# Kernel tuning notes

Hardware: AMD Instinct MI355X
Metric: run time of the kernel (lower is better)

Reference implementation:

```python
import jax, jax.numpy as jnp
import numpy as np

N, E, D, H, LAYERS = 50000, 800000, 128, 8, 2
LRELU_ALPHA = 0.2


def _seg_softmax(logits, seg, n):
    # numerically stable softmax over edges grouped by destination node
    m = jax.ops.segment_max(logits, seg, num_segments=n)
    z = jnp.exp(logits - m[seg])
    s = jax.ops.segment_sum(z, seg, num_segments=n)
    return z / jnp.maximum(s[seg], 1e-16)


def _gat_layer(x, src, dst, W, a_src, a_dst, concat):
    # W: [H, Fin, F'], a_src/a_dst: [H, F']
    n = x.shape[0]
    outs = []
    for h in range(W.shape[0]):  # loop over heads to bound peak memory
        Wh = x @ W[h]                              # [N, F']
        es = Wh @ a_src[h]                         # [N]
        ed = Wh @ a_dst[h]                         # [N]
        e = jax.nn.leaky_relu(es[src] + ed[dst], LRELU_ALPHA)  # [E]
        att = _seg_softmax(e, dst, n)              # [E]
        out = jax.ops.segment_sum(att[:, None] * Wh[src], dst, num_segments=n)
        outs.append(out)
    if concat:
        return jax.nn.elu(jnp.concatenate(outs, axis=-1))  # [N, H*F']
    return jnp.mean(jnp.stack(outs, axis=0), axis=0)        # [N, F']


def _rel_gcn_layer(x, src, dst, w, W):
    # weighted-adjacency GCN with row (in-degree) normalization + ReLU
    n = x.shape[0]
    deg = jax.ops.segment_sum(w, dst, num_segments=n)
    norm = w / jnp.maximum(deg[dst], 1e-16)        # [E]
    h = x @ W                                      # [N, Dout]
    agg = jax.ops.segment_sum(norm[:, None] * h[src], dst, num_segments=n)
    return jax.nn.relu(agg)


def setup_inputs() -> dict:
    key = jax.random.key(0)
    ks = jax.random.split(key, 12)
    s = 1.0 / np.sqrt(D)
    return {
        "x": jax.random.normal(ks[0], (N, D), dtype=jnp.float32),
        "edge_index": jax.random.randint(ks[1], (2, E), 0, N, dtype=jnp.int64),
        "edge_weight": jax.random.uniform(ks[2], (E,), dtype=jnp.float32),
        "gat_W0": jax.random.normal(ks[3], (H, D, D // H), dtype=jnp.float32) * s,
        "gat_a0_src": jax.random.normal(ks[4], (H, D // H), dtype=jnp.float32) * s,
        "gat_a0_dst": jax.random.normal(ks[5], (H, D // H), dtype=jnp.float32) * s,
        "gat_W1": jax.random.normal(ks[6], (H, D, D), dtype=jnp.float32) * s,
        "gat_a1_src": jax.random.normal(ks[7], (H, D), dtype=jnp.float32) * s,
        "gat_a1_dst": jax.random.normal(ks[8], (H, D), dtype=jnp.float32) * s,
        "gcn_W0": jax.random.normal(ks[9], (D, D), dtype=jnp.float32) * s,
        "gcn_W1": jax.random.normal(ks[10], (D, D), dtype=jnp.float32) * s,
    }


def reference(x, edge_index, edge_weight, gat_W0, gat_a0_src, gat_a0_dst,
              gat_W1, gat_a1_src, gat_a1_dst, gcn_W0, gcn_W1):
    src, dst = edge_index[0], edge_index[1]
    gat_params = [(gat_W0, gat_a0_src, gat_a0_dst), (gat_W1, gat_a1_src, gat_a1_dst)]
    gcn_params = [gcn_W0, gcn_W1]
    x1, x2 = x, x  # dropout is identity in eval mode
    for i in range(LAYERS):
        W, a_s, a_d = gat_params[i]
        x1 = _gat_layer(x1, src, dst, W, a_s, a_d, concat=(i != LAYERS - 1))
        x2 = _rel_gcn_layer(x2, src, dst, edge_weight, gcn_params[i])
    # cat along new last dim then MaxPool1d(2) == elementwise max of branches
    return jnp.maximum(x1, x2)
```

## Files before the change

### kernel.cpp

```cpp
#include <hip/hip_runtime.h>

#define LRELU_ALPHA 0.2f

typedef __attribute__((ext_vector_type(8))) short short8;
typedef __attribute__((ext_vector_type(4))) float float4v;
typedef __attribute__((ext_vector_type(2))) float f32x2;

__device__ __forceinline__ unsigned short f2bf(float f) {
  union { float f; unsigned u; } x; x.f = f;
  unsigned r = (x.u + 0x7fff + ((x.u >> 16) & 1)) >> 16;
  return (unsigned short)r;
}
__device__ __forceinline__ float bflo(unsigned u) {
  union { unsigned u; float f; } x; x.u = u << 16; return x.f;
}
__device__ __forceinline__ float bfhi(unsigned u) {
  union { unsigned u; float f; } x; x.u = u & 0xffff0000u; return x.f;
}
__device__ __forceinline__ f32x2 bfpair(unsigned u) {
  return (f32x2){bflo(u), bfhi(u)};
}
__device__ __forceinline__ unsigned packbf(float a, float b) {
  return (unsigned)f2bf(a) | ((unsigned)f2bf(b) << 16);
}


__global__ __launch_bounds__(256) void k_count(const int* __restrict__ dst,
                                               int* __restrict__ cnt, int E) {
  int e = blockIdx.x * 256 + threadIdx.x;
  if (e < E) atomicAdd(&cnt[dst[e]], 1);
}

__global__ __launch_bounds__(1024) void k_scan1(const int* __restrict__ cnt,
                                                int* __restrict__ lscan,
                                                int* __restrict__ bsum, int N) {
  __shared__ int sm[1024];
  int t = threadIdx.x;
  int base = blockIdx.x * 1024;
  int v = (base + t < N) ? cnt[base + t] : 0;
  sm[t] = v;
  __syncthreads();
  for (int off = 1; off < 1024; off <<= 1) {
    int x = (t >= off) ? sm[t - off] : 0;
    __syncthreads();
    sm[t] += x;
    __syncthreads();
  }
  if (base + t < N) lscan[base + t] = sm[t] - v;
  if (t == 1023) bsum[blockIdx.x] = sm[1023];
}

__global__ __launch_bounds__(64) void k_scan2(int* __restrict__ bsum,
                                              int* __restrict__ rowptrN, int nb) {
  int t = threadIdx.x;
  int v = (t < nb) ? bsum[t] : 0;
  int orig = v;
  for (int off = 1; off < 64; off <<= 1) {
    int y = __shfl_up(v, off, 64);
    if (t >= off) v += y;
  }
  if (t < nb) bsum[t] = v - orig;
  if (t == 63) *rowptrN = v;
}

__global__ __launch_bounds__(1024) void k_scan3(int* __restrict__ rowptr,
                                                int* __restrict__ cur,
                                                const int* __restrict__ bsum, int N) {
  int i = blockIdx.x * 1024 + threadIdx.x;
  if (i < N) {
    int v = rowptr[i] + bsum[blockIdx.x];
    rowptr[i] = v;
    cur[i] = v;
  }
}

__global__ __launch_bounds__(256) void k_scatter(const int* __restrict__ src,
                                                 const int* __restrict__ dst,
                                                 const float* __restrict__ w,
                                                 const float* __restrict__ logit0,
                                                 int* __restrict__ cur,
                                                 uint2* __restrict__ edata,
                                                 unsigned short* __restrict__ pedge,
                                                 int E) {
  int e = blockIdx.x * 256 + threadIdx.x;
  if (e >= E) return;
  int d = dst[e];
  int s = src[e];
  int p = atomicAdd(&cur[d], 1);
  edata[p] = make_uint2((unsigned)s, __float_as_uint(w[e]));
  float4 es0 = *(const float4*)(logit0 + (size_t)s * 16);
  float4 es1 = *(const float4*)(logit0 + (size_t)s * 16 + 4);
  float4 ed0 = *(const float4*)(logit0 + (size_t)d * 16 + 8);
  float4 ed1 = *(const float4*)(logit0 + (size_t)d * 16 + 12);
  float lg[8] = {es0.x + ed0.x, es0.y + ed0.y, es0.z + ed0.z, es0.w + ed0.w,
                 es1.x + ed1.x, es1.y + ed1.y, es1.z + ed1.z, es1.w + ed1.w};
  unsigned short o[8];
#pragma unroll
  for (int h = 0; h < 8; ++h) {
    float v = lg[h] > 0.f ? lg[h] : LRELU_ALPHA * lg[h];
    o[h] = f2bf(__expf(fminf(v, 80.f)));
  }
  ushort4 q0 = {o[0], o[1], o[2], o[3]};
  ushort4 q1 = {o[4], o[5], o[6], o[7]};
  *(ushort4*)(pedge + (size_t)p * 8) = q0;
  *(ushort4*)(pedge + (size_t)p * 8 + 4) = q1;
}

__global__ __launch_bounds__(256) void k_pack(const float* __restrict__ W0,
                                              const float* __restrict__ a0s,
                                              const float* __restrict__ a0d,
                                              const float* __restrict__ W1,
                                              const float* __restrict__ a1s,
                                              const float* __restrict__ a1d,
                                              const float* __restrict__ gw0,
                                              const float* __restrict__ gw1,
                                              unsigned short* __restrict__ W0catT,
                                              float* __restrict__ logitW,
                                              unsigned short* __restrict__ gw1T,
                                              unsigned short* __restrict__ va1T,
                                              unsigned short* __restrict__ WstackT) {
  int idx = blockIdx.x * 256 + threadIdx.x;
  if (idx < 32768) {
    int n = idx >> 7, k = idx & 127;
    int q = n >> 2, r = n & 3;
    float v;
    if (r < 2) {
      int o = 2 * q + r;
      int h = o >> 4, f = o & 15;
      v = W0[h * 2048 + k * 16 + f];
    } else {
      int j = 2 * q + (r - 2);
      v = gw0[k * 128 + j];
    }
    W0catT[idx] = f2bf(v);
  } else if (idx < 34816) {
    int j = idx - 32768;
    int k = j >> 4, c = j & 15;
    int h = (c < 8) ? c : c - 8;
    const float* a = (c < 8) ? a0s : a0d;
    float s = 0.f;
    for (int f = 0; f < 16; ++f) s += W0[h * 2048 + k * 16 + f] * a[h * 16 + f];
    logitW[j] = s;
  } else if (idx < 51200) {
    int j = idx - 34816;
    int n = j >> 7, k = j & 127;
    gw1T[j] = f2bf(gw1[k * 128 + n]);
  } else if (idx < 53248) {
    int j = idx - 51200;
    int c = j >> 7, k = j & 127;
    int h = c & 7;
    const float* a = (c < 8) ? a1s : a1d;
    float s = 0.f;
    for (int f = 0; f < 128; ++f) s += W1[h * 16384 + k * 128 + f] * a[h * 128 + f];
    va1T[j] = f2bf(s);
  } else if (idx < 184320) {
    int j = idx - 53248;
    int n = j >> 10, kk = j & 1023;
    int h = kk >> 7, k = kk & 127;
    WstackT[j] = f2bf(W1[h * 16384 + k * 128 + n] * 0.125f);
  }
}

__global__ __launch_bounds__(256) void k_prep(const float* __restrict__ x,
                                              const float* __restrict__ logitW,
                                              unsigned short* __restrict__ xb,
                                              float* __restrict__ logit0, int N) {
  __shared__ float sm[16][132];
  __shared__ float sw[2048];
  int t = threadIdx.x;
  int base = blockIdx.x * 16;
  int r = t >> 4, cc = (t & 15) * 8;
  const float* xr = x + (size_t)(base + r) * 128 + cc;
  float4 v0 = *(const float4*)xr;
  float4 v1 = *(const float4*)(xr + 4);
  ushort4 o0 = {f2bf(v0.x), f2bf(v0.y), f2bf(v0.z), f2bf(v0.w)};
  ushort4 o1 = {f2bf(v1.x), f2bf(v1.y), f2bf(v1.z), f2bf(v1.w)};
  *(ushort4*)(xb + (size_t)(base + r) * 128 + cc) = o0;
  *(ushort4*)(xb + (size_t)(base + r) * 128 + cc + 4) = o1;
  *(float4*)&sm[r][cc] = v0;
  *(float4*)&sm[r][cc + 4] = v1;
  *(float4*)&sw[t * 8] = *(const float4*)(logitW + t * 8);
  *(float4*)&sw[t * 8 + 4] = *(const float4*)(logitW + t * 8 + 4);
  __syncthreads();
  int c = t & 15;
  float acc = 0.f;
#pragma unroll
  for (int k = 0; k < 128; ++k) acc += sm[r][k] * sw[k * 16 + c];
  logit0[(size_t)(base + r) * 16 + c] = acc;
}

__global__ __launch_bounds__(256) void k_pedge(const float* __restrict__ logits,
                                               const uint2* __restrict__ edata,
                                               const int* __restrict__ rowptr,
                                               unsigned short* __restrict__ pedge,
                                               float* __restrict__ linv, int N) {
  int wave = threadIdx.x >> 6, lane = threadIdx.x & 63;
  int d = blockIdx.x * 4 + wave;
  if (d >= N) return;
  int j8 = lane >> 3, h = lane & 7;
  float edv = logits[(size_t)d * 16 + 8 + h];
  int beg = rowptr[d], end = rowptr[d + 1];
  float lsum = 0.f;
  for (int ii = beg + j8; ii < end; ii += 8) {
    unsigned s = edata[ii].x;
    float es = logits[(size_t)s * 16 + h];
    float lg = es + edv;
    lg = lg > 0.f ? lg : LRELU_ALPHA * lg;
    float p = __expf(fminf(lg, 80.f));
    lsum += p;
    pedge[(size_t)ii * 8 + h] = f2bf(p);
  }
  lsum += __shfl_xor(lsum, 8, 64);
  lsum += __shfl_xor(lsum, 16, 64);
  lsum += __shfl_xor(lsum, 32, 64);
  if (lane < 8) linv[(size_t)d * 8 + h] = lsum > 0.f ? 1.f / lsum : 0.f;
}

template <int NT, int OUT_BF16, int EPI>
__global__ __launch_bounds__(256) void k_mgemm(const unsigned short* __restrict__ A, int lda,
                                               const unsigned short* __restrict__ BT, int ldb,
                                               void* __restrict__ Cv, int ldc,
                                               const void* __restrict__ aux,
                                               int M, int Ncols, int K) {
  __shared__ unsigned short As[64][64];
  __shared__ unsigned short Bs[NT * 16][64];
  int tid = threadIdx.x;
  int w = tid >> 6, lane = tid & 63;
  int quad = lane >> 4, l16 = lane & 15;
  int row0 = blockIdx.x * 64;
  int c0 = blockIdx.y * (NT * 16);
  float4v acc[NT];
#pragma unroll
  for (int t = 0; t < NT; ++t) acc[t] = (float4v){0.f, 0.f, 0.f, 0.f};

  for (int k0 = 0; k0 < K; k0 += 64) {
    __syncthreads();
#pragma unroll
    for (int i = 0; i < 2; ++i) {
      int c = tid + i * 256;
      int r = c >> 3, kc = c & 7;
      uint4 v = {0u, 0u, 0u, 0u};
      int gr = row0 + r;
      if (gr < M) v = *(const uint4*)(A + (size_t)gr * lda + k0 + kc * 8);
      *(uint4*)(&As[r][(kc ^ (r & 7)) * 8]) = v;
    }
#pragma unroll
    for (int i = 0; i < (NT * 128 + 255) / 256; ++i) {
      int c = tid + i * 256;
      if (c < NT * 128) {
        int n = c >> 3, kc = c & 7;
        uint4 v = {0u, 0u, 0u, 0u};
        int gn = c0 + n;
        if (gn < Ncols) v = *(const uint4*)(BT + (size_t)gn * ldb + k0 + kc * 8);
        *(uint4*)(&Bs[n][(kc ^ (n & 7)) * 8]) = v;
      }
    }
    __syncthreads();
#pragma unroll
    for (int ks = 0; ks < 2; ++ks) {
      int m = w * 16 + l16;
      int ga = (ks * 4 + quad) ^ (m & 7);
      short8 a = *(const short8*)(&As[m][ga * 8]);
#pragma unroll
      for (int t = 0; t < NT; ++t) {
        int n = t * 16 + l16;
        int gb = (ks * 4 + quad) ^ (n & 7);
        short8 b = *(const short8*)(&Bs[n][gb * 8]);
        acc[t] = __builtin_amdgcn_mfma_f32_16x16x32_bf16(a, b, acc[t], 0, 0, 0);
      }
    }
  }
#pragma unroll
  for (int t = 0; t < NT; ++t) {
    int cc = c0 + t * 16 + l16;
    if (cc >= Ncols) continue;
#pragma unroll
    for (int i = 0; i < 4; ++i) {
      int rr = row0 + w * 16 + quad * 4 + i;
      if (rr >= M) continue;
      float v = acc[t][i];
      if (EPI == 1) {
        unsigned short us = ((const unsigned short*)aux)[(size_t)rr * ldc + cc];
        v = fmaxf(v, bflo((unsigned)us));
      }
      if (EPI == 2) {
        ((unsigned short*)Cv)[(size_t)rr * 256 + 4 * (cc >> 1) + 2 + (cc & 1)] = f2bf(v);
      } else if (EPI == 3) {
        int enc = __builtin_amdgcn_cvt_pk_fp8_f32(v, v, 0, false);
        ((unsigned char*)Cv)[(size_t)rr * ldc + cc] = (unsigned char)(enc & 0xff);
      } else if (OUT_BF16)
        ((unsigned short*)Cv)[(size_t)rr * ldc + cc] = f2bf(v);
      else
        ((float*)Cv)[(size_t)rr * ldc + cc] = v;
    }
  }
}

__global__ __launch_bounds__(256) void k_agg0(const unsigned char* __restrict__ feat8,
                                              const int* __restrict__ rowptr,
                                              const uint2* __restrict__ edata,
                                              const unsigned short* __restrict__ pedge,
                                              unsigned short* __restrict__ x1c,
                                              unsigned short* __restrict__ x2,
                                              unsigned short* __restrict__ xh, int N) {
  __shared__ uint2 swl[4][64];
  __shared__ float pl[4][512];
  int wave = threadIdx.x >> 6, lane = threadIdx.x & 63;
  int d = blockIdx.x * 4 + wave;
  if (d >= N) return;
  int half = lane >> 5, lane2 = lane & 31;
  int head = lane2 >> 2;
  int beg = rowptr[d], end = rowptr[d + 1], deg = end - beg;
  f32x2 aa = {0.f, 0.f}, ab = {0.f, 0.f}, ga = {0.f, 0.f}, gb = {0.f, 0.f};
  float l = 0.f, wsum = 0.f;
  for (int base = 0; base < deg; base += 64) {
    int idx = beg + base + lane;
    uint2 sv = make_uint2(0u, 0u);
    uint4 q = make_uint4(0u, 0u, 0u, 0u);
    if (idx < end) {
      sv = edata[idx];
      q = *(const uint4*)(pedge + (size_t)idx * 8);
    }
    swl[wave][lane] = sv;
    float4 pa = make_float4(bflo(q.x), bfhi(q.x), bflo(q.y), bfhi(q.y));
    float4 pb = make_float4(bflo(q.z), bfhi(q.z), bflo(q.w), bfhi(q.w));
    *(float4*)&pl[wave][lane * 8] = pa;
    *(float4*)&pl[wave][lane * 8 + 4] = pb;
    int ng = deg - base; if (ng > 64) ng = 64;
    int tp = (ng + 1) >> 1;
    int t = 0;
    for (; t + 2 <= tp; t += 2) {
      int e0 = 2 * t + half, e1 = e0 + 2;
      uint2 sw0 = swl[wave][e0], sw1 = swl[wave][e1];
      float p0 = pl[wave][e0 * 8 + head], p1 = pl[wave][e1 * 8 + head];
      uint2 u0 = *(const uint2*)(feat8 + (size_t)sw0.x * 256 + 8 * lane2);
      uint2 u1 = *(const uint2*)(feat8 + (size_t)sw1.x * 256 + 8 * lane2);
      float w0 = __uint_as_float(sw0.y), w1 = __uint_as_float(sw1.y);
      f32x2 gA0 = __builtin_amdgcn_cvt_pk_f32_fp8(u0.x, false);
      f32x2 cA0 = __builtin_amdgcn_cvt_pk_f32_fp8(u0.x, true);
      f32x2 gB0 = __builtin_amdgcn_cvt_pk_f32_fp8(u0.y, false);
      f32x2 cB0 = __builtin_amdgcn_cvt_pk_f32_fp8(u0.y, true);
      aa += gA0 * p0; ga += cA0 * w0; ab += gB0 * p0; gb += cB0 * w0;
      l += p0; wsum += w0;
      f32x2 gA1 = __builtin_amdgcn_cvt_pk_f32_fp8(u1.x, false);
      f32x2 cA1 = __builtin_amdgcn_cvt_pk_f32_fp8(u1.x, true);
      f32x2 gB1 = __builtin_amdgcn_cvt_pk_f32_fp8(u1.y, false);
      f32x2 cB1 = __builtin_amdgcn_cvt_pk_f32_fp8(u1.y, true);
      aa += gA1 * p1; ga += cA1 * w1; ab += gB1 * p1; gb += cB1 * w1;
      l += p1; wsum += w1;
    }
    for (; t < tp; ++t) {
      int e = 2 * t + half;
      uint2 sw = swl[wave][e];
      float p = pl[wave][e * 8 + head];
      float wj = __uint_as_float(sw.y);
      uint2 u = *(const uint2*)(feat8 + (size_t)sw.x * 256 + 8 * lane2);
      f32x2 gA = __builtin_amdgcn_cvt_pk_f32_fp8(u.x, false);
      f32x2 cA = __builtin_amdgcn_cvt_pk_f32_fp8(u.x, true);
      f32x2 gB = __builtin_amdgcn_cvt_pk_f32_fp8(u.y, false);
      f32x2 cB = __builtin_amdgcn_cvt_pk_f32_fp8(u.y, true);
      aa += gA * p; ga += cA * wj; ab += gB * p; gb += cB * wj;
      l += p; wsum += wj;
    }
  }
  aa.x += __shfl_xor(aa.x, 32, 64); aa.y += __shfl_xor(aa.y, 32, 64);
  ab.x += __shfl_xor(ab.x, 32, 64); ab.y += __shfl_xor(ab.y, 32, 64);
  ga.x += __shfl_xor(ga.x, 32, 64); ga.y += __shfl_xor(ga.y, 32, 64);
  gb.x += __shfl_xor(gb.x, 32, 64); gb.y += __shfl_xor(gb.y, 32, 64);
  l += __shfl_xor(l, 32, 64);
  wsum += __shfl_xor(wsum, 32, 64);
  if (half == 0) {
    float inv = l > 0.f ? 1.f / l : 0.f;
    float v0 = aa.x * inv, v1 = aa.y * inv, v2 = ab.x * inv, v3 = ab.y * inv;
    v0 = v0 > 0.f ? v0 : __expf(v0) - 1.f;
    v1 = v1 > 0.f ? v1 : __expf(v1) - 1.f;
    v2 = v2 > 0.f ? v2 : __expf(v2) - 1.f;
    v3 = v3 > 0.f ? v3 : __expf(v3) - 1.f;
    unsigned p0 = packbf(v0, v1), p1 = packbf(v2, v3);
    ((uint2*)x1c)[(size_t)d * 32 + lane2] = make_uint2(p0, p1);
    ((unsigned*)xh)[(size_t)d * 128 + 4 * lane2] = p0;
    ((unsigned*)xh)[(size_t)d * 128 + 4 * lane2 + 2] = p1;
    float ginv = 1.f / fmaxf(wsum, 1e-16f);
    float w0 = fmaxf(ga.x * ginv, 0.f), w1 = fmaxf(ga.y * ginv, 0.f);
    float w2 = fmaxf(gb.x * ginv, 0.f), w3 = fmaxf(gb.y * ginv, 0.f);
    ((uint2*)x2)[(size_t)d * 32 + lane2] = make_uint2(packbf(w0, w1), packbf(w2, w3));
  }
}

__global__ __launch_bounds__(256) void k_agg1(const unsigned short* __restrict__ xh,
                                              const int* __restrict__ rowptr,
                                              const uint2* __restrict__ edata,
                                              const unsigned short* __restrict__ pedge,
                                              const float* __restrict__ linv,
                                              unsigned short* __restrict__ aggbuf,
                                              unsigned short* __restrict__ x2f,
                                              int d0, int d1) {
  __shared__ uint2 swl[4][64];
  __shared__ float pl[4][512];
  int wave = threadIdx.x >> 6, lane = threadIdx.x & 63;
  int d = d0 + blockIdx.x * 4 + wave;
  if (d >= d1) return;
  int half = lane >> 5, lane2 = lane & 31;
  int beg = rowptr[d], end = rowptr[d + 1], deg = end - beg;
  f32x2 axA[8] = {}, axB[8] = {};
  f32x2 ga = {0.f, 0.f}, gb = {0.f, 0.f};
  float wsum = 0.f;
  for (int base = 0; base < deg; base += 64) {
    int idx = beg + base + lane;
    uint2 sv = make_uint2(0u, 0u);
    uint4 q = make_uint4(0u, 0u, 0u, 0u);
    if (idx < end) {
      sv = edata[idx];
      q = *(const uint4*)(pedge + (size_t)idx * 8);
    }
    swl[wave][lane] = sv;
    float4 pa = make_float4(bflo(q.x), bfhi(q.x), bflo(q.y), bfhi(q.y));
    float4 pb = make_float4(bflo(q.z), bfhi(q.z), bflo(q.w), bfhi(q.w));
    *(float4*)&pl[wave][lane * 8] = pa;
    *(float4*)&pl[wave][lane * 8 + 4] = pb;
    int ng = deg - base; if (ng > 64) ng = 64;
    int tp = (ng + 1) >> 1;
    for (int t = 0; t < tp; ++t) {
      int e = 2 * t + half;
      uint2 sw = swl[wave][e];
      float4 pv0 = *(const float4*)&pl[wave][e * 8];
      float4 pv1 = *(const float4*)&pl[wave][e * 8 + 4];
      float wj = __uint_as_float(sw.y);
      uint4 u = *(const uint4*)(xh + (size_t)sw.x * 256 + 8 * lane2);
      f32x2 xA = bfpair(u.x), hA = bfpair(u.y);
      f32x2 xB = bfpair(u.z), hB = bfpair(u.w);
      ga += hA * wj;
      gb += hB * wj;
      wsum += wj;
      axA[0] += xA * pv0.x; axB[0] += xB * pv0.x;
      axA[1] += xA * pv0.y; axB[1] += xB * pv0.y;
      axA[2] += xA * pv0.z; axB[2] += xB * pv0.z;
      axA[3] += xA * pv0.w; axB[3] += xB * pv0.w;
      axA[4] += xA * pv1.x; axB[4] += xB * pv1.x;
      axA[5] += xA * pv1.y; axB[5] += xB * pv1.y;
      axA[6] += xA * pv1.z; axB[6] += xB * pv1.z;
      axA[7] += xA * pv1.w; axB[7] += xB * pv1.w;
    }
  }
#pragma unroll
  for (int h = 0; h < 8; ++h) {
    axA[h].x += __shfl_xor(axA[h].x, 32, 64); axA[h].y += __shfl_xor(axA[h].y, 32, 64);
    axB[h].x += __shfl_xor(axB[h].x, 32, 64); axB[h].y += __shfl_xor(axB[h].y, 32, 64);
  }
  ga.x += __shfl_xor(ga.x, 32, 64); ga.y += __shfl_xor(ga.y, 32, 64);
  gb.x += __shfl_xor(gb.x, 32, 64); gb.y += __shfl_xor(gb.y, 32, 64);
  wsum += __shfl_xor(wsum, 32, 64);
  if (half == 0) {
    float4 i0 = *(const float4*)(linv + (size_t)d * 8);
    float4 i1 = *(const float4*)(linv + (size_t)d * 8 + 4);
    float invh[8] = {i0.x, i0.y, i0.z, i0.w, i1.x, i1.y, i1.z, i1.w};
    size_t lr2 = (size_t)(d - d0) * 256;
#pragma unroll
    for (int h = 0; h < 8; ++h) {
      ((uint2*)aggbuf)[lr2 + h * 32 + lane2] =
          make_uint2(packbf(axA[h].x * invh[h], axA[h].y * invh[h]),
                     packbf(axB[h].x * invh[h], axB[h].y * invh[h]));
    }
    float ginv = 1.f / fmaxf(wsum, 1e-16f);
    float w0 = fmaxf(ga.x * ginv, 0.f), w1 = fmaxf(ga.y * ginv, 0.f);
    float w2 = fmaxf(gb.x * ginv, 0.f), w3 = fmaxf(gb.y * ginv, 0.f);
    ((uint2*)x2f)[(size_t)d * 32 + lane2] = make_uint2(packbf(w0, w1), packbf(w2, w3));
  }
}


extern "C" void kernel_launch(void* const* d_in, const int* in_sizes, int n_in,
                              void* d_out, int out_size, void* d_ws, size_t ws_size,
                              hipStream_t stream) {
  const float* x   = (const float*)d_in[0];
  const int*   ei  = (const int*)d_in[1];
  const float* ew  = (const float*)d_in[2];
  const float* W0  = (const float*)d_in[3];
  const float* a0s = (const float*)d_in[4];
  const float* a0d = (const float*)d_in[5];
  const float* W1  = (const float*)d_in[6];
  const float* a1s = (const float*)d_in[7];
  const float* a1d = (const float*)d_in[8];
  const float* gw0 = (const float*)d_in[9];
  const float* gw1 = (const float*)d_in[10];
  float* out = (float*)d_out;

  const int N = in_sizes[0] / 128;
  const int E = in_sizes[1] / 2;
  const int* src = ei;
  const int* dst = ei + E;

  char* p = (char*)d_ws;
  auto carve = [&](size_t bytes) {
    void* r = (void*)p;
    p += (bytes + 255) & ~(size_t)255;
    return r;
  };
  int*   cnt    = (int*)carve((size_t)N * 4);
  int*   rowptr = (int*)carve((size_t)(N + 1) * 4);
  int*   cur    = (int*)carve((size_t)N * 4);
  int*   bsum   = (int*)carve(256 * 4);
  uint2* edata  = (uint2*)carve((size_t)E * 8);
  unsigned short* W0catT  = (unsigned short*)carve(32768 * 2);
  float*          logitW  = (float*)carve(2048 * 4);
  unsigned short* gw1T    = (unsigned short*)carve(16384 * 2);
  unsigned short* va1T    = (unsigned short*)carve(2048 * 2);
  unsigned short* WstackT = (unsigned short*)carve(131072 * 2);
  unsigned short* x1c  = (unsigned short*)carve((size_t)N * 128 * 2);
  unsigned short* x2   = (unsigned short*)carve((size_t)N * 128 * 2);
  unsigned short* x2f  = (unsigned short*)carve((size_t)N * 128 * 2);
  float*          esed = (float*)carve((size_t)N * 16 * 4);
  unsigned short* xh   = (unsigned short*)carve((size_t)N * 256 * 2);
  unsigned short* pedge = (unsigned short*)carve((size_t)E * 8 * 2);
  float*          linv1 = (float*)carve((size_t)N * 8 * 4);
  const int CH = 25600;
  size_t ph1 = ((size_t)N * 128 * 2 + 255) & ~(size_t)255;
  size_t ph2 = ph1 + (((size_t)N * 256 + 255) & ~(size_t)255);
  size_t ph3 = ph2 + (((size_t)N * 16 * 4 + 255) & ~(size_t)255);
  size_t scratch_sz = (size_t)CH * 1024 * 2;
  if (ph3 > scratch_sz) scratch_sz = ph3;
  char* scratch = (char*)carve(scratch_sz);
  unsigned short* xb     = (unsigned short*)scratch;
  unsigned char*  feat8  = (unsigned char*)(scratch + ph1);
  float*          logit0 = (float*)(scratch + ph2);
  unsigned short* aggbuf = (unsigned short*)scratch;

  int gE = (E + 255) / 256;
  int nb = (N + 1023) / 1024;
  int gM = (N + 63) / 64;
  int gD = (N + 3) / 4;

  hipMemsetAsync(cnt, 0, (size_t)N * 4, stream);
  k_count<<<gE, 256, 0, stream>>>(dst, cnt, E);
  k_scan1<<<nb, 1024, 0, stream>>>(cnt, rowptr, bsum, N);
  k_scan2<<<1, 64, 0, stream>>>(bsum, rowptr + N, nb);
  k_scan3<<<nb, 1024, 0, stream>>>(rowptr, cur, bsum, N);

  k_pack<<<(184320 + 255) / 256, 256, 0, stream>>>(W0, a0s, a0d, W1, a1s, a1d, gw0,
                                                   gw1, W0catT, logitW, gw1T, va1T,
                                                   WstackT);
  k_prep<<<(N + 15) / 16, 256, 0, stream>>>(x, logitW, xb, logit0, N);

  k_scatter<<<gE, 256, 0, stream>>>(src, dst, ew, logit0, cur, edata, pedge, E);

  k_mgemm<8, 1, 3><<<dim3(gM, 2), 256, 0, stream>>>(xb, 128, W0catT, 128, feat8, 256,
                                                    nullptr, N, 256, 128);
  k_agg0<<<gD, 256, 0, stream>>>(feat8, rowptr, edata, pedge, x1c, x2, xh, N);

  k_mgemm<1, 0, 0><<<dim3(gM, 1), 256, 0, stream>>>(x1c, 128, va1T, 128, esed, 16,
                                                    nullptr, N, 16, 128);
  k_mgemm<8, 1, 2><<<dim3(gM, 1), 256, 0, stream>>>(x2, 128, gw1T, 128, xh, 256,
                                                    nullptr, N, 128, 128);

  k_pedge<<<gD, 256, 0, stream>>>(esed, edata, rowptr, pedge, linv1, N);

  for (int d0 = 0; d0 < N; d0 += CH) {
    int d1 = d0 + CH < N ? d0 + CH : N;
    int chN = d1 - d0;
    k_agg1<<<(chN + 3) / 4, 256, 0, stream>>>(xh, rowptr, edata, pedge, linv1,
                                              aggbuf, x2f, d0, d1);
    k_mgemm<8, 0, 1><<<dim3((chN + 63) / 64, 1), 256, 0, stream>>>(
        aggbuf, 1024, WstackT, 1024, out + (size_t)d0 * 128, 128,
        x2f + (size_t)d0 * 128, chN, 128, 1024);
  }
}
```

Measured before the change: 464.1 us.

## Split layer-0 features into bf16 GAT and fp8 GCN buffers, batch scatter, unchunk layer 1

```diff
diff --git a/kernel.cpp b/kernel.cpp
--- a/kernel.cpp
+++ b/kernel.cpp
@@ -82,28 +82,46 @@
                                                  uint2* __restrict__ edata,
                                                  unsigned short* __restrict__ pedge,
                                                  int E) {
-  int e = blockIdx.x * 256 + threadIdx.x;
-  if (e >= E) return;
-  int d = dst[e];
-  int s = src[e];
-  int p = atomicAdd(&cur[d], 1);
-  edata[p] = make_uint2((unsigned)s, __float_as_uint(w[e]));
-  float4 es0 = *(const float4*)(logit0 + (size_t)s * 16);
-  float4 es1 = *(const float4*)(logit0 + (size_t)s * 16 + 4);
-  float4 ed0 = *(const float4*)(logit0 + (size_t)d * 16 + 8);
-  float4 ed1 = *(const float4*)(logit0 + (size_t)d * 16 + 12);
-  float lg[8] = {es0.x + ed0.x, es0.y + ed0.y, es0.z + ed0.z, es0.w + ed0.w,
-                 es1.x + ed1.x, es1.y + ed1.y, es1.z + ed1.z, es1.w + ed1.w};
-  unsigned short o[8];
-#pragma unroll
-  for (int h = 0; h < 8; ++h) {
-    float v = lg[h] > 0.f ? lg[h] : LRELU_ALPHA * lg[h];
-    o[h] = f2bf(__expf(fminf(v, 80.f)));
-  }
-  ushort4 q0 = {o[0], o[1], o[2], o[3]};
-  ushort4 q1 = {o[4], o[5], o[6], o[7]};
-  *(ushort4*)(pedge + (size_t)p * 8) = q0;
-  *(ushort4*)(pedge + (size_t)p * 8 + 4) = q1;
+  int base = (blockIdx.x * 256 + threadIdx.x) * 4;
+  if (base >= E) return;
+  int n = E - base; if (n > 4) n = 4;
+  int ss[4], dd[4]; float ww[4];
+  if (n == 4) {
+    int4 s4 = *(const int4*)(src + base);
+    int4 d4 = *(const int4*)(dst + base);
+    float4 w4 = *(const float4*)(w + base);
+    ss[0] = s4.x; ss[1] = s4.y; ss[2] = s4.z; ss[3] = s4.w;
+    dd[0] = d4.x; dd[1] = d4.y; dd[2] = d4.z; dd[3] = d4.w;
+    ww[0] = w4.x; ww[1] = w4.y; ww[2] = w4.z; ww[3] = w4.w;
+  } else {
+    for (int i = 0; i < n; ++i) { ss[i] = src[base + i]; dd[i] = dst[base + i]; ww[i] = w[base + i]; }
+  }
+  int pp[4];
+#pragma unroll
+  for (int i = 0; i < 4; ++i)
+    if (i < n) pp[i] = atomicAdd(&cur[dd[i]], 1);
+#pragma unroll
+  for (int i = 0; i < 4; ++i) {
+    if (i >= n) break;
+    int s = ss[i], d = dd[i], p = pp[i];
+    edata[p] = make_uint2((unsigned)s, __float_as_uint(ww[i]));
+    float4 es0 = *(const float4*)(logit0 + (size_t)s * 16);
+    float4 es1 = *(const float4*)(logit0 + (size_t)s * 16 + 4);
+    float4 ed0 = *(const float4*)(logit0 + (size_t)d * 16 + 8);
+    float4 ed1 = *(const float4*)(logit0 + (size_t)d * 16 + 12);
+    float lg[8] = {es0.x + ed0.x, es0.y + ed0.y, es0.z + ed0.z, es0.w + ed0.w,
+                   es1.x + ed1.x, es1.y + ed1.y, es1.z + ed1.z, es1.w + ed1.w};
+    unsigned short o[8];
+#pragma unroll
+    for (int h = 0; h < 8; ++h) {
+      float v = lg[h] > 0.f ? lg[h] : LRELU_ALPHA * lg[h];
+      o[h] = f2bf(__expf(fminf(v, 80.f)));
+    }
+    ushort4 q0 = {o[0], o[1], o[2], o[3]};
+    ushort4 q1 = {o[4], o[5], o[6], o[7]};
+    *(ushort4*)(pedge + (size_t)p * 8) = q0;
+    *(ushort4*)(pedge + (size_t)p * 8 + 4) = q1;
+  }
 }
 
 __global__ __launch_bounds__(256) void k_pack(const float* __restrict__ W0,
@@ -122,15 +140,12 @@
   int idx = blockIdx.x * 256 + threadIdx.x;
   if (idx < 32768) {
     int n = idx >> 7, k = idx & 127;
-    int q = n >> 2, r = n & 3;
     float v;
-    if (r < 2) {
-      int o = 2 * q + r;
-      int h = o >> 4, f = o & 15;
+    if (n < 128) {
+      int h = n >> 4, f = n & 15;
       v = W0[h * 2048 + k * 16 + f];
     } else {
-      int j = 2 * q + (r - 2);
-      v = gw0[k * 128 + j];
+      v = gw0[k * 128 + (n - 128)];
     }
     W0catT[idx] = f2bf(v);
   } else if (idx < 34816) {
@@ -285,9 +300,13 @@
       }
       if (EPI == 2) {
         ((unsigned short*)Cv)[(size_t)rr * 256 + 4 * (cc >> 1) + 2 + (cc & 1)] = f2bf(v);
-      } else if (EPI == 3) {
-        int enc = __builtin_amdgcn_cvt_pk_fp8_f32(v, v, 0, false);
-        ((unsigned char*)Cv)[(size_t)rr * ldc + cc] = (unsigned char)(enc & 0xff);
+      } else if (EPI == 4) {
+        if (cc < 128) {
+          ((unsigned short*)Cv)[(size_t)rr * 128 + cc] = f2bf(v);
+        } else {
+          int enc = __builtin_amdgcn_cvt_pk_fp8_f32(v, v, 0, false);
+          ((unsigned char*)aux)[(size_t)rr * 128 + (cc - 128)] = (unsigned char)(enc & 0xff);
+        }
       } else if (OUT_BF16)
         ((unsigned short*)Cv)[(size_t)rr * ldc + cc] = f2bf(v);
       else
@@ -296,7 +315,8 @@
   }
 }
 
-__global__ __launch_bounds__(256) void k_agg0(const unsigned char* __restrict__ feat8,
+__global__ __launch_bounds__(256) void k_agg0(const unsigned short* __restrict__ featg,
+                                              const unsigned char* __restrict__ featc,
                                               const int* __restrict__ rowptr,
                                               const uint2* __restrict__ edata,
                                               const unsigned short* __restrict__ pedge,
@@ -333,20 +353,20 @@
       int e0 = 2 * t + half, e1 = e0 + 2;
       uint2 sw0 = swl[wave][e0], sw1 = swl[wave][e1];
       float p0 = pl[wave][e0 * 8 + head], p1 = pl[wave][e1 * 8 + head];
-      uint2 u0 = *(const uint2*)(feat8 + (size_t)sw0.x * 256 + 8 * lane2);
-      uint2 u1 = *(const uint2*)(feat8 + (size_t)sw1.x * 256 + 8 * lane2);
+      uint2 g0 = ((const uint2*)featg)[(size_t)sw0.x * 32 + lane2];
+      unsigned c0v = ((const unsigned*)featc)[(size_t)sw0.x * 32 + lane2];
+      uint2 g1 = ((const uint2*)featg)[(size_t)sw1.x * 32 + lane2];
+      unsigned c1v = ((const unsigned*)featc)[(size_t)sw1.x * 32 + lane2];
       float w0 = __uint_as_float(sw0.y), w1 = __uint_as_float(sw1.y);
-      f32x2 gA0 = __builtin_amdgcn_cvt_pk_f32_fp8(u0.x, false);
-      f32x2 cA0 = __builtin_amdgcn_cvt_pk_f32_fp8(u0.x, true);
-      f32x2 gB0 = __builtin_amdgcn_cvt_pk_f32_fp8(u0.y, false);
-      f32x2 cB0 = __builtin_amdgcn_cvt_pk_f32_fp8(u0.y, true);
-      aa += gA0 * p0; ga += cA0 * w0; ab += gB0 * p0; gb += cB0 * w0;
+      aa += bfpair(g0.x) * p0;
+      ab += bfpair(g0.y) * p0;
+      ga += __builtin_amdgcn_cvt_pk_f32_fp8(c0v, false) * w0;
+      gb += __builtin_amdgcn_cvt_pk_f32_fp8(c0v, true) * w0;
       l += p0; wsum += w0;
-      f32x2 gA1 = __builtin_amdgcn_cvt_pk_f32_fp8(u1.x, false);
-      f32x2 cA1 = __builtin_amdgcn_cvt_pk_f32_fp8(u1.x, true);
-      f32x2 gB1 = __builtin_amdgcn_cvt_pk_f32_fp8(u1.y, false);
-      f32x2 cB1 = __builtin_amdgcn_cvt_pk_f32_fp8(u1.y, true);
-      aa += gA1 * p1; ga += cA1 * w1; ab += gB1 * p1; gb += cB1 * w1;
+      aa += bfpair(g1.x) * p1;
+      ab += bfpair(g1.y) * p1;
+      ga += __builtin_amdgcn_cvt_pk_f32_fp8(c1v, false) * w1;
+      gb += __builtin_amdgcn_cvt_pk_f32_fp8(c1v, true) * w1;
       l += p1; wsum += w1;
     }
     for (; t < tp; ++t) {
@@ -354,12 +374,12 @@
       uint2 sw = swl[wave][e];
       float p = pl[wave][e * 8 + head];
       float wj = __uint_as_float(sw.y);
-      uint2 u = *(const uint2*)(feat8 + (size_t)sw.x * 256 + 8 * lane2);
-      f32x2 gA = __builtin_amdgcn_cvt_pk_f32_fp8(u.x, false);
-      f32x2 cA = __builtin_amdgcn_cvt_pk_f32_fp8(u.x, true);
-      f32x2 gB = __builtin_amdgcn_cvt_pk_f32_fp8(u.y, false);
-      f32x2 cB = __builtin_amdgcn_cvt_pk_f32_fp8(u.y, true);
-      aa += gA * p; ga += cA * wj; ab += gB * p; gb += cB * wj;
+      uint2 g = ((const uint2*)featg)[(size_t)sw.x * 32 + lane2];
+      unsigned cv = ((const unsigned*)featc)[(size_t)sw.x * 32 + lane2];
+      aa += bfpair(g.x) * p;
+      ab += bfpair(g.y) * p;
+      ga += __builtin_amdgcn_cvt_pk_f32_fp8(cv, false) * wj;
+      gb += __builtin_amdgcn_cvt_pk_f32_fp8(cv, true) * wj;
       l += p; wsum += wj;
     }
   }
@@ -393,13 +413,12 @@
                                               const unsigned short* __restrict__ pedge,
                                               const float* __restrict__ linv,
                                               unsigned short* __restrict__ aggbuf,
-                                              unsigned short* __restrict__ x2f,
-                                              int d0, int d1) {
+                                              unsigned short* __restrict__ x2f, int N) {
   __shared__ uint2 swl[4][64];
   __shared__ float pl[4][512];
   int wave = threadIdx.x >> 6, lane = threadIdx.x & 63;
-  int d = d0 + blockIdx.x * 4 + wave;
-  if (d >= d1) return;
+  int d = blockIdx.x * 4 + wave;
+  if (d >= N) return;
   int half = lane >> 5, lane2 = lane & 31;
   int beg = rowptr[d], end = rowptr[d + 1], deg = end - beg;
   f32x2 axA[8] = {}, axB[8] = {};
@@ -454,7 +473,7 @@
     float4 i0 = *(const float4*)(linv + (size_t)d * 8);
     float4 i1 = *(const float4*)(linv + (size_t)d * 8 + 4);
     float invh[8] = {i0.x, i0.y, i0.z, i0.w, i1.x, i1.y, i1.z, i1.w};
-    size_t lr2 = (size_t)(d - d0) * 256;
+    size_t lr2 = (size_t)d * 256;
 #pragma unroll
     for (int h = 0; h < 8; ++h) {
       ((uint2*)aggbuf)[lr2 + h * 32 + lane2] =
@@ -506,26 +525,28 @@
   unsigned short* gw1T    = (unsigned short*)carve(16384 * 2);
   unsigned short* va1T    = (unsigned short*)carve(2048 * 2);
   unsigned short* WstackT = (unsigned short*)carve(131072 * 2);
-  unsigned short* x1c  = (unsigned short*)carve((size_t)N * 128 * 2);
   unsigned short* x2   = (unsigned short*)carve((size_t)N * 128 * 2);
-  unsigned short* x2f  = (unsigned short*)carve((size_t)N * 128 * 2);
   float*          esed = (float*)carve((size_t)N * 16 * 4);
   unsigned short* xh   = (unsigned short*)carve((size_t)N * 256 * 2);
   unsigned short* pedge = (unsigned short*)carve((size_t)E * 8 * 2);
   float*          linv1 = (float*)carve((size_t)N * 8 * 4);
-  const int CH = 25600;
   size_t ph1 = ((size_t)N * 128 * 2 + 255) & ~(size_t)255;
-  size_t ph2 = ph1 + (((size_t)N * 256 + 255) & ~(size_t)255);
-  size_t ph3 = ph2 + (((size_t)N * 16 * 4 + 255) & ~(size_t)255);
-  size_t scratch_sz = (size_t)CH * 1024 * 2;
-  if (ph3 > scratch_sz) scratch_sz = ph3;
+  size_t ph2 = ph1 + (((size_t)N * 128 * 2 + 255) & ~(size_t)255);
+  size_t ph3 = ph2 + (((size_t)N * 128 + 255) & ~(size_t)255);
+  size_t ph4 = ph3 + (((size_t)N * 16 * 4 + 255) & ~(size_t)255);
+  size_t scratch_sz = (size_t)N * 1024 * 2;
+  if (ph4 > scratch_sz) scratch_sz = ph4;
   char* scratch = (char*)carve(scratch_sz);
   unsigned short* xb     = (unsigned short*)scratch;
-  unsigned char*  feat8  = (unsigned char*)(scratch + ph1);
-  float*          logit0 = (float*)(scratch + ph2);
+  unsigned short* x1c    = (unsigned short*)scratch;
+  unsigned short* featg  = (unsigned short*)(scratch + ph1);
+  unsigned char*  featc  = (unsigned char*)(scratch + ph2);
+  float*          logit0 = (float*)(scratch + ph3);
   unsigned short* aggbuf = (unsigned short*)scratch;
+  unsigned short* x2f    = x2;
 
   int gE = (E + 255) / 256;
+  int gE4 = ((E + 3) / 4 + 255) / 256;
   int nb = (N + 1023) / 1024;
   int gM = (N + 63) / 64;
   int gD = (N + 3) / 4;
@@ -541,11 +562,11 @@
                                                    WstackT);
   k_prep<<<(N + 15) / 16, 256, 0, stream>>>(x, logitW, xb, logit0, N);
 
-  k_scatter<<<gE, 256, 0, stream>>>(src, dst, ew, logit0, cur, edata, pedge, E);
-
-  k_mgemm<8, 1, 3><<<dim3(gM, 2), 256, 0, stream>>>(xb, 128, W0catT, 128, feat8, 256,
-                                                    nullptr, N, 256, 128);
-  k_agg0<<<gD, 256, 0, stream>>>(feat8, rowptr, edata, pedge, x1c, x2, xh, N);
+  k_scatter<<<gE4, 256, 0, stream>>>(src, dst, ew, logit0, cur, edata, pedge, E);
+
+  k_mgemm<8, 1, 4><<<dim3(gM, 2), 256, 0, stream>>>(xb, 128, W0catT, 128, featg, 128,
+                                                    featc, N, 256, 128);
+  k_agg0<<<gD, 256, 0, stream>>>(featg, featc, rowptr, edata, pedge, x1c, x2, xh, N);
 
   k_mgemm<1, 0, 0><<<dim3(gM, 1), 256, 0, stream>>>(x1c, 128, va1T, 128, esed, 16,
                                                     nullptr, N, 16, 128);
@@ -554,13 +575,8 @@
 
   k_pedge<<<gD, 256, 0, stream>>>(esed, edata, rowptr, pedge, linv1, N);
 
-  for (int d0 = 0; d0 < N; d0 += CH) {
-    int d1 = d0 + CH < N ? d0 + CH : N;
-    int chN = d1 - d0;
-    k_agg1<<<(chN + 3) / 4, 256, 0, stream>>>(xh, rowptr, edata, pedge, linv1,
-                                              aggbuf, x2f, d0, d1);
-    k_mgemm<8, 0, 1><<<dim3((chN + 63) / 64, 1), 256, 0, stream>>>(
-        aggbuf, 1024, WstackT, 1024, out + (size_t)d0 * 128, 128,
-        x2f + (size_t)d0 * 128, chN, 128, 1024);
-  }
-}
+  k_agg1<<<gD, 256, 0, stream>>>(xh, rowptr, edata, pedge, linv1, aggbuf, x2f, N);
+
+  k_mgemm<8, 0, 1><<<dim3(gM, 1), 256, 0, stream>>>(aggbuf, 1024, WstackT, 1024, out,
+                                                    128, x2f, N, 128, 1024);
+}
```

Measured after the change: 451.4 us. 1.03x faster.
